# Performance work log

Measured on AMD Instinct MI355X. Metric: run time of the kernel, lower is better.

## Reference

```python
import jax, jax.numpy as jnp
import numpy as np

BIGNET_DIM = 1024
N_LAYERS = 18   # 6 blocks * 3 QLoRALinear
N_LN = 5
GROUPS = 64     # 1024 / group_size(16)
GS = 16
RANK = 32
BATCH = 16384
EPS = 1e-5


def dequant(qw, scale):
    # qw: [O, G, gs] int 0..15, scale: [O, G] per-group max-abs norm
    w = (qw.astype(jnp.float32) / 15.0 * 2.0 - 1.0) * scale[..., None]
    return w.reshape(qw.shape[0], -1)  # [O, I]


def qlora_linear(x, qw, scale, b, a_w, b_w):
    w = dequant(qw, scale)                      # [O, I]
    base = x @ w.T + b                          # [N, O]
    lora = (x @ a_w.T) @ b_w.T                  # [N, r] @ [r, O]
    return base + lora


def layernorm(h, g, b):
    mu = h.mean(-1, keepdims=True)
    var = jnp.mean((h - mu) ** 2, -1, keepdims=True)
    return (h - mu) * jax.lax.rsqrt(var + EPS) * g + b


def setup_inputs() -> dict:
    key = jax.random.key(0)
    ks = jax.random.split(key, 8)
    x = jax.random.normal(ks[0], (BATCH, BIGNET_DIM), jnp.float32)
    qw = jax.random.randint(ks[1], (N_LAYERS, BIGNET_DIM, GROUPS, GS), 0, 16, jnp.int32)
    scale = jax.random.uniform(ks[2], (N_LAYERS, BIGNET_DIM, GROUPS), jnp.float32) * 0.05
    bias = jax.random.normal(ks[3], (N_LAYERS, BIGNET_DIM), jnp.float32) * 0.02
    la = jax.random.normal(ks[4], (N_LAYERS, RANK, BIGNET_DIM), jnp.float32) * (2.0 / BIGNET_DIM) ** 0.5
    # note: torch zero-inits lora_b; use small random values so the LoRA path is testable
    lb = jax.random.normal(ks[5], (N_LAYERS, BIGNET_DIM, RANK), jnp.float32) * 0.01
    ln_w = jnp.ones((N_LN, BIGNET_DIM), jnp.float32)
    ln_b = jnp.zeros((N_LN, BIGNET_DIM), jnp.float32)
    return {"x": x, "scale": scale, "bias": bias, "la": la, "lb": lb,
            "ln_w": ln_w, "ln_b": ln_b, "qw": qw}


def reference(x, scale, bias, la, lb, ln_w, ln_b, qw):
    h = x
    li = 0
    for blk in range(6):
        r = h
        for j in range(3):
            h = qlora_linear(h, qw[li], scale[li], bias[li], la[li], lb[li])
            li += 1
            if j < 2:
                h = jax.nn.relu(h)
        h = h + r
        if blk < 5:
            h = layernorm(h, ln_w[blk], ln_b[blk])
    return h
```

## Files before the change

kernel.cpp:

```cpp
#include <hip/hip_runtime.h>

typedef unsigned short UST;
typedef __attribute__((ext_vector_type(8))) __bf16 bf16x8;
typedef __attribute__((ext_vector_type(4))) float f32x4;

__device__ __forceinline__ float bf2f(UST u) {
    union { unsigned int i; float f; } v; v.i = ((unsigned int)u) << 16; return v.f;
}
__device__ __forceinline__ UST f2bf(float f) {
    union { float f; unsigned int i; } v; v.f = f;
    return (UST)((v.i + 0x7fffu + ((v.i >> 16) & 1u)) >> 16);
}

__device__ __forceinline__ void gl2lds16(const UST* g, UST* l) {
    __builtin_amdgcn_global_load_lds(
        (const __attribute__((address_space(1))) unsigned int*)g,
        (__attribute__((address_space(3))) unsigned int*)l, 16, 0, 0);
}

#define WBAR8 asm volatile("s_waitcnt vmcnt(8)\n\ts_barrier" ::: "memory")
#define WBAR4 asm volatile("s_waitcnt vmcnt(4)\n\ts_barrier" ::: "memory")
#define WBAR0 asm volatile("s_waitcnt vmcnt(0)\n\ts_barrier" ::: "memory")
#define BAR   asm volatile("s_barrier" ::: "memory")
#define LGB   asm volatile("s_waitcnt lgkmcnt(0)\n\ts_barrier" ::: "memory")
#define LGW   do { asm volatile("s_waitcnt lgkmcnt(0)" ::: "memory"); \
                   __builtin_amdgcn_sched_barrier(0); } while (0)

__global__ __launch_bounds__(256) void prep_w(
    const int* __restrict__ qw, const float* __restrict__ scale,
    const float* __restrict__ la, const float* __restrict__ lb,
    UST* __restrict__ wp)
{
    int l = blockIdx.x, ot = blockIdx.y, it = blockIdx.z;
    __shared__ float buf[8192];
    __shared__ float sc_s[128 * 8];
    int t = threadIdx.x;
    int wave = t >> 6, lane = t & 63;
    int wm = wave >> 1, wn = wave & 1;
    int la15 = lane & 15, qa = lane >> 4;

    {
        int e = t * 4;
        int o = e >> 3, g = e & 7;
        const float* sb = scale + ((size_t)l * 1024 + ot * 128 + o) * 64 + it * 8 + g;
        *(float4*)&sc_s[e] = *(const float4*)sb;
    }

    float* last = buf;
    {
        const float* laB = la + (size_t)l * 32 * 1024 + it * 128;
        #pragma unroll
        for (int p = 0; p < 4; p++) {
            int e = t * 4 + p * 1024;
            int r = e >> 7, i0 = e & 127;
            float4 v = *(const float4*)(laB + (size_t)r * 1024 + i0);
            last[(i0 + 0) * 33 + r] = v.x;
            last[(i0 + 1) * 33 + r] = v.y;
            last[(i0 + 2) * 33 + r] = v.z;
            last[(i0 + 3) * 33 + r] = v.w;
        }
    }

    bf16x8 af[4];
    const float* lbL = lb + ((size_t)l * 1024 + ot * 128 + wm * 64 + la15) * 32 + qa * 8;
    #pragma unroll
    for (int mi = 0; mi < 4; mi++) {
        float4 u0 = *(const float4*)(lbL + mi * 16 * 32);
        float4 u1 = *(const float4*)(lbL + mi * 16 * 32 + 4);
        union { bf16x8 v; UST u[8]; } A;
        A.u[0] = f2bf(u0.x); A.u[1] = f2bf(u0.y); A.u[2] = f2bf(u0.z); A.u[3] = f2bf(u0.w);
        A.u[4] = f2bf(u1.x); A.u[5] = f2bf(u1.y); A.u[6] = f2bf(u1.z); A.u[7] = f2bf(u1.w);
        af[mi] = A.v;
    }

    __syncthreads();

    bf16x8 bfr[4];
    #pragma unroll
    for (int ni = 0; ni < 4; ni++) {
        int iloc = wn * 64 + ni * 16 + la15;
        const float* pp = &last[iloc * 33 + qa * 8];
        union { bf16x8 v; UST u[8]; } B;
        #pragma unroll
        for (int j = 0; j < 8; j++) B.u[j] = f2bf(pp[j]);
        bfr[ni] = B.v;
    }

    f32x4 acc[4][4];
    #pragma unroll
    for (int mi = 0; mi < 4; mi++)
        #pragma unroll
        for (int ni = 0; ni < 4; ni++) {
            acc[mi][ni] = (f32x4){0.f, 0.f, 0.f, 0.f};
            acc[mi][ni] = __builtin_amdgcn_mfma_f32_16x16x32_bf16(
                af[mi], bfr[ni], acc[mi][ni], 0, 0, 0);
        }

    __syncthreads();

    float* cs = buf;
    int cc = t & 15, rw = t >> 4;
    UST* wL = wp + (size_t)l * 1048576;
    const int* qL = qw + (size_t)l * 1048576;
    #pragma unroll
    for (int h = 0; h < 2; ++h) {
        int4 qd[4][2];
        #pragma unroll
        for (int g = 0; g < 4; g++) {
            int rl = g * 16 + rw;
            const int* qrow = qL + (size_t)(ot * 128 + h * 64 + rl) * 1024
                              + it * 128 + cc * 8;
            qd[g][0] = *(const int4*)qrow;
            qd[g][1] = *(const int4*)(qrow + 4);
        }
        if (wm == h) {
            #pragma unroll
            for (int mi = 0; mi < 4; mi++)
                #pragma unroll
                for (int ni = 0; ni < 4; ni++) {
                    int colx = (wn * 64 + ni * 16 + la15) ^ (qa << 4);
                    #pragma unroll
                    for (int r2 = 0; r2 < 4; r2++) {
                        int rl = mi * 16 + qa * 4 + r2;
                        cs[rl * 128 + colx] = acc[mi][ni][r2];
                    }
                }
        }
        LGB;
        #pragma unroll
        for (int g = 0; g < 4; ++g) {
            int rl = g * 16 + rw;
            int swz = ((rl >> 2) & 3) << 2;
            int gr0 = ((cc * 2) ^ swz) * 4;
            float4 v0 = *(const float4*)&cs[rl * 128 + gr0];
            float4 v1 = *(const float4*)&cs[rl * 128 + gr0 + 4];
            float s = sc_s[(h * 64 + rl) * 8 + (cc >> 1)];
            float t2 = s * (2.0f / 15.0f);
            float o0 = fmaf((float)qd[g][0].x, t2, v0.x - s);
            float o1 = fmaf((float)qd[g][0].y, t2, v0.y - s);
            float o2 = fmaf((float)qd[g][0].z, t2, v0.z - s);
            float o3 = fmaf((float)qd[g][0].w, t2, v0.w - s);
            float o4 = fmaf((float)qd[g][1].x, t2, v1.x - s);
            float o5 = fmaf((float)qd[g][1].y, t2, v1.y - s);
            float o6 = fmaf((float)qd[g][1].z, t2, v1.z - s);
            float o7 = fmaf((float)qd[g][1].w, t2, v1.w - s);
            uint4 pk;
            pk.x = (unsigned)f2bf(o0) | ((unsigned)f2bf(o1) << 16);
            pk.y = (unsigned)f2bf(o2) | ((unsigned)f2bf(o3) << 16);
            pk.z = (unsigned)f2bf(o4) | ((unsigned)f2bf(o5) << 16);
            pk.w = (unsigned)f2bf(o6) | ((unsigned)f2bf(o7) << 16);
            *(uint4*)&wL[(size_t)(ot * 128 + h * 64 + rl) * 1024 + it * 128 + cc * 8] = pk;
        }
        LGB;
    }
}

__global__ __launch_bounds__(256) void f32_to_bf16(const float* __restrict__ x,
                                                   UST* __restrict__ o)
{
    size_t i = ((size_t)blockIdx.x * 256 + threadIdx.x) * 4;
    float4 v = *(const float4*)(x + i);
    *(ushort4*)(o + i) = make_ushort4(f2bf(v.x), f2bf(v.y), f2bf(v.z), f2bf(v.w));
}

#define BK 32

__global__ __launch_bounds__(512, 2) void gemm_ep(
    const UST* __restrict__ X, const UST* __restrict__ W,
    const float* __restrict__ bias,
    UST* __restrict__ outb, const UST* __restrict__ resid,
    float* __restrict__ outf, int mode)
{
    const int K = 1024;
    __shared__ UST smem[65536];
    int tid = threadIdx.x;
    int wave = tid >> 6, lane = tid & 63;
    int wm = wave >> 2, wn = wave & 3;
    int la15 = lane & 15, qa = lane >> 4;

    int bid = blockIdx.x;
    int xcd = bid & 7, idx = bid >> 3;
    int bm = xcd * 8 + (idx & 7);
    int bn = idx >> 3;

    int c0 = tid, c1 = tid + 512;
    int r0 = c0 >> 2, k0c = ((c0 & 3) ^ ((r0 >> 1) & 3)) * 8;
    int r1 = c1 >> 2, k1c = ((c1 & 3) ^ ((r1 >> 1) & 3)) * 8;
    const UST* gA0 = X + (size_t)(bm * 256 + r0) * K + k0c;
    const UST* gA1 = X + (size_t)(bm * 256 + r1) * K + k1c;
    const UST* gB0 = W + (size_t)(bn * 256 + r0) * K + k0c;
    const UST* gB1 = W + (size_t)(bn * 256 + r1) * K + k1c;

    int offA[8], offB[4];
    #pragma unroll
    for (int i = 0; i < 8; i++) {
        int ra = wm * 128 + i * 16 + la15;
        offA[i] = ra * 32 + ((qa ^ ((ra >> 1) & 3)) * 8);
    }
    #pragma unroll
    for (int i = 0; i < 4; i++) {
        int rb = wn * 64 + i * 16 + la15;
        offB[i] = rb * 32 + ((qa ^ ((rb >> 1) & 3)) * 8);
    }

    f32x4 acc[8][4];
    #pragma unroll
    for (int i = 0; i < 8; i++)
        #pragma unroll
        for (int j = 0; j < 4; j++) acc[i][j] = (f32x4){0.f, 0.f, 0.f, 0.f};

    auto stageA = [&](int s) {
        UST* sA = smem + (s & 3) * 16384;
        gl2lds16(gA0 + s * BK, sA + c0 * 8);
        gl2lds16(gA1 + s * BK, sA + c1 * 8);
    };
    auto stageB = [&](int s) {
        UST* sB = smem + (s & 3) * 16384 + 8192;
        gl2lds16(gB0 + s * BK, sB + c0 * 8);
        gl2lds16(gB1 + s * BK, sB + c1 * 8);
    };

    stageA(0); stageB(0);
    stageA(1); stageB(1);
    stageA(2); stageB(2);

#define STEPBODY(s, WAITM, DOST)                                            \
    {                                                                       \
        const UST* pA = smem + ((s) & 3) * 16384;                           \
        const UST* pB = pA + 8192;                                          \
        WAITM;                                             \
        bf16x8 af0[4], bfn[4];                                              \
        _Pragma("unroll")                                                   \
        for (int mi = 0; mi < 4; mi++) af0[mi] = *(const bf16x8*)&pA[offA[mi]]; \
        _Pragma("unroll")                                                   \
        for (int ni = 0; ni < 4; ni++) bfn[ni] = *(const bf16x8*)&pB[offB[ni]]; \
        if (DOST) stageA((s) + 3);                                          \
        LGW;                                                                \
        __builtin_amdgcn_s_setprio(1);                                      \
        _Pragma("unroll")                                                   \
        for (int mi = 0; mi < 4; mi++)                                      \
            _Pragma("unroll")                                               \
            for (int ni = 0; ni < 4; ni++)                                  \
                acc[mi][ni] = __builtin_amdgcn_mfma_f32_16x16x32_bf16(      \
                    af0[mi], bfn[ni], acc[mi][ni], 0, 0, 0);                \
        __builtin_amdgcn_s_setprio(0);                                      \
        BAR;                                                                \
        bf16x8 af1[4];                                                      \
        _Pragma("unroll")                                                   \
        for (int mi = 0; mi < 4; mi++) af1[mi] = *(const bf16x8*)&pA[offA[4 + mi]]; \
        if (DOST) stageB((s) + 3);                                          \
        LGW;                                                                \
        __builtin_amdgcn_s_setprio(1);                                      \
        _Pragma("unroll")                                                   \
        for (int mi = 0; mi < 4; mi++)                                      \
            _Pragma("unroll")                                               \
            for (int ni = 0; ni < 4; ni++)                                  \
                acc[4 + mi][ni] = __builtin_amdgcn_mfma_f32_16x16x32_bf16(  \
                    af1[mi], bfn[ni], acc[4 + mi][ni], 0, 0, 0);            \
        __builtin_amdgcn_s_setprio(0);                                      \
    }

    for (int s = 0; s < 29; ++s) STEPBODY(s, WBAR8, 1);
    STEPBODY(29, WBAR8, 0);
    STEPBODY(30, WBAR4, 0);
    STEPBODY(31, WBAR0, 0);
#undef STEPBODY
    LGB;

    float* cs = (float*)smem;
    int cc = tid & 31, rw = tid >> 5;
    int gcolb = bn * 256 + cc * 8;
    float4 bv0 = *(const float4*)&bias[gcolb];
    float4 bv1 = *(const float4*)&bias[gcolb + 4];

    #pragma unroll
    for (int h = 0; h < 4; ++h) {
        if (wm == (h >> 1)) {
            #pragma unroll
            for (int m = 0; m < 4; m++) {
                int mi = (h & 1) * 4 + m;
                #pragma unroll
                for (int ni = 0; ni < 4; ni++) {
                    int colx = (wn * 64 + ni * 16 + la15) ^ (qa << 4);
                    #pragma unroll
                    for (int r2 = 0; r2 < 4; r2++) {
                        int rl = m * 16 + qa * 4 + r2;
                        cs[rl * 256 + colx] = acc[mi][ni][r2];
                    }
                }
            }
        }
        LGB;
        #pragma unroll
        for (int g = 0; g < 4; ++g) {
            int rl = g * 16 + rw;
            int swz = ((rl >> 2) & 3) << 2;
            int gr0 = ((cc * 2) ^ swz) * 4;
            float4 v0 = *(const float4*)&cs[rl * 256 + gr0];
            float4 v1 = *(const float4*)&cs[rl * 256 + gr0 + 4];
            float o0 = v0.x + bv0.x, o1 = v0.y + bv0.y;
            float o2 = v0.z + bv0.z, o3 = v0.w + bv0.w;
            float o4 = v1.x + bv1.x, o5 = v1.y + bv1.y;
            float o6 = v1.z + bv1.z, o7 = v1.w + bv1.w;
            if (mode == 0) {
                o0 = fmaxf(o0, 0.f); o1 = fmaxf(o1, 0.f);
                o2 = fmaxf(o2, 0.f); o3 = fmaxf(o3, 0.f);
                o4 = fmaxf(o4, 0.f); o5 = fmaxf(o5, 0.f);
                o6 = fmaxf(o6, 0.f); o7 = fmaxf(o7, 0.f);
            }
            int grow = bm * 256 + h * 64 + rl;
            size_t base = (size_t)grow * 1024 + gcolb;
            if (mode != 0) {
                ushort4 rv0 = *(const ushort4*)&resid[base];
                ushort4 rv1 = *(const ushort4*)&resid[base + 4];
                o0 += bf2f(rv0.x); o1 += bf2f(rv0.y);
                o2 += bf2f(rv0.z); o3 += bf2f(rv0.w);
                o4 += bf2f(rv1.x); o5 += bf2f(rv1.y);
                o6 += bf2f(rv1.z); o7 += bf2f(rv1.w);
            }
            if (mode == 2) {
                *(float4*)&outf[base] = make_float4(o0, o1, o2, o3);
                *(float4*)&outf[base + 4] = make_float4(o4, o5, o6, o7);
            } else {
                uint4 pk;
                pk.x = (unsigned)f2bf(o0) | ((unsigned)f2bf(o1) << 16);
                pk.y = (unsigned)f2bf(o2) | ((unsigned)f2bf(o3) << 16);
                pk.z = (unsigned)f2bf(o4) | ((unsigned)f2bf(o5) << 16);
                pk.w = (unsigned)f2bf(o6) | ((unsigned)f2bf(o7) << 16);
                *(uint4*)&outb[base] = pk;
            }
        }
        LGB;
    }
}

__global__ __launch_bounds__(256) void ln_only(
    const UST* __restrict__ s, UST* __restrict__ r,
    const float* __restrict__ g, const float* __restrict__ b)
{
    int wave = threadIdx.x >> 6, lane = threadIdx.x & 63;
    int row = blockIdx.x * 4 + wave;
    const UST* sp = s + (size_t)row * 1024;
    UST* rp = r + (size_t)row * 1024;

    float v[16];
    float sum = 0.f, ss = 0.f;
    #pragma unroll
    for (int k = 0; k < 4; k++) {
        ushort4 hv = *(const ushort4*)(sp + k * 256 + lane * 4);
        float a0 = bf2f(hv.x), a1 = bf2f(hv.y), a2 = bf2f(hv.z), a3 = bf2f(hv.w);
        v[k * 4 + 0] = a0; v[k * 4 + 1] = a1; v[k * 4 + 2] = a2; v[k * 4 + 3] = a3;
        sum += a0 + a1 + a2 + a3;
        ss += a0 * a0 + a1 * a1 + a2 * a2 + a3 * a3;
    }
    #pragma unroll
    for (int off = 32; off > 0; off >>= 1) {
        sum += __shfl_down(sum, off, 64);
        ss  += __shfl_down(ss, off, 64);
    }
    sum = __shfl(sum, 0, 64);
    ss  = __shfl(ss, 0, 64);
    float mean = sum * (1.0f / 1024.0f);
    float var = ss * (1.0f / 1024.0f) - mean * mean;
    float rstd = rsqrtf(var + 1e-5f);

    #pragma unroll
    for (int k = 0; k < 4; k++) {
        int c = k * 256 + lane * 4;
        float4 gv = *(const float4*)(g + c);
        float4 bv = *(const float4*)(b + c);
        ushort4 o;
        o.x = f2bf((v[k * 4 + 0] - mean) * rstd * gv.x + bv.x);
        o.y = f2bf((v[k * 4 + 1] - mean) * rstd * gv.y + bv.y);
        o.z = f2bf((v[k * 4 + 2] - mean) * rstd * gv.z + bv.z);
        o.w = f2bf((v[k * 4 + 3] - mean) * rstd * gv.w + bv.w);
        *(ushort4*)(rp + c) = o;
    }
}

extern "C" void kernel_launch(void* const* d_in, const int* in_sizes, int n_in,
                              void* d_out, int out_size, void* d_ws, size_t ws_size,
                              hipStream_t stream) {
    const float* x     = (const float*)d_in[0];
    const float* scale = (const float*)d_in[1];
    const float* bias  = (const float*)d_in[2];
    const float* la    = (const float*)d_in[3];
    const float* lb    = (const float*)d_in[4];
    const float* ln_w  = (const float*)d_in[5];
    const float* ln_b  = (const float*)d_in[6];
    const int*   qw    = (const int*)d_in[7];

    const int M = in_sizes[0] / 1024;
    const size_t WPB = (size_t)18 * 1024 * 1024 * 2;
    const size_t ACT = (size_t)M * 1024 * 2;

    UST* wp = (UST*)d_ws;
    UST* A  = (UST*)((char*)d_ws + WPB);
    UST* Cb = (UST*)((char*)d_ws + WPB + ACT);
    UST* Bb = (UST*)d_out;

    prep_w<<<dim3(18, 8, 8), 256, 0, stream>>>(qw, scale, la, lb, wp);
    f32_to_bf16<<<(M * 1024) / (256 * 4), 256, 0, stream>>>(x, A);

    int nblk = (M / 256) * 4;
    int li = 0;
    for (int blk = 0; blk < 6; ++blk) {
        gemm_ep<<<nblk, 512, 0, stream>>>(
            A, wp + (size_t)li * 1024 * 1024, bias + li * 1024, Bb, nullptr, nullptr, 0);
        li++;
        gemm_ep<<<nblk, 512, 0, stream>>>(
            Bb, wp + (size_t)li * 1024 * 1024, bias + li * 1024, Cb, nullptr, nullptr, 0);
        li++;
        if (blk < 5) {
            gemm_ep<<<nblk, 512, 0, stream>>>(
                Cb, wp + (size_t)li * 1024 * 1024, bias + li * 1024, Bb, A, nullptr, 1);
            li++;
            ln_only<<<M / 4, 256, 0, stream>>>(Bb, A, ln_w + blk * 1024, ln_b + blk * 1024);
        } else {
            gemm_ep<<<nblk, 512, 0, stream>>>(
                Cb, wp + (size_t)li * 1024 * 1024, bias + li * 1024, nullptr, A,
                (float*)d_out, 2);
            li++;
        }
    }
}
```

Baseline: 929.9 us.

## Prefetch next-stage LDS fragments into double-buffered registers during GEMM main loop

Restructures the GEMM main loop so that the B fragments and first half of the A fragments for the next K-step are read from LDS into ping-pong register sets while the current step's second MFMA half runs. All four global-to-LDS copies for a stage are now issued together, and the per-step barrier count drops from two to one at the end of each step. The goal is to hide LDS read latency behind MFMAs and cut synchronisation. In exchange it raises register pressure and makes the wait counts more delicate, since the loads for step s+3 now target the buffer just read in step s-1.

Result: slower. 1.035 ms (+11.3%).

```diff
diff --git a/kernel.cpp b/kernel.cpp
--- a/kernel.cpp
+++ b/kernel.cpp
@@ -18,10 +18,9 @@
         (__attribute__((address_space(3))) unsigned int*)l, 16, 0, 0);
 }
 
-#define WBAR8 asm volatile("s_waitcnt vmcnt(8)\n\ts_barrier" ::: "memory")
 #define WBAR4 asm volatile("s_waitcnt vmcnt(4)\n\ts_barrier" ::: "memory")
 #define WBAR0 asm volatile("s_waitcnt vmcnt(0)\n\ts_barrier" ::: "memory")
-#define BAR   asm volatile("s_barrier" ::: "memory")
+#define WNONE do {} while (0)
 #define LGB   asm volatile("s_waitcnt lgkmcnt(0)\n\ts_barrier" ::: "memory")
 #define LGW   do { asm volatile("s_waitcnt lgkmcnt(0)" ::: "memory"); \
                    __builtin_amdgcn_sched_barrier(0); } while (0)
@@ -209,63 +208,73 @@
         #pragma unroll
         for (int j = 0; j < 4; j++) acc[i][j] = (f32x4){0.f, 0.f, 0.f, 0.f};
 
-    auto stageA = [&](int s) {
-        UST* sA = smem + (s & 3) * 16384;
-        gl2lds16(gA0 + s * BK, sA + c0 * 8);
-        gl2lds16(gA1 + s * BK, sA + c1 * 8);
+    auto stage = [&](int s) {
+        UST* d = smem + (s & 3) * 16384;
+        gl2lds16(gA0 + s * BK, d + c0 * 8);
+        gl2lds16(gA1 + s * BK, d + c1 * 8);
+        gl2lds16(gB0 + s * BK, d + 8192 + c0 * 8);
+        gl2lds16(gB1 + s * BK, d + 8192 + c1 * 8);
     };
-    auto stageB = [&](int s) {
-        UST* sB = smem + (s & 3) * 16384 + 8192;
-        gl2lds16(gB0 + s * BK, sB + c0 * 8);
-        gl2lds16(gB1 + s * BK, sB + c1 * 8);
-    };
-
-    stageA(0); stageB(0);
-    stageA(1); stageB(1);
-    stageA(2); stageB(2);
-
-#define STEPBODY(s, WAITM, DOST)                                            \
+
+    bf16x8 bfA[4], af0A[4], bfB[4], af0B[4];
+
+    stage(0); stage(1); stage(2);
+    WBAR4;
+    {
+        const UST* pA = smem;
+        const UST* pB = pA + 8192;
+        #pragma unroll
+        for (int i = 0; i < 4; i++) bfA[i] = *(const bf16x8*)&pB[offB[i]];
+        #pragma unroll
+        for (int i = 0; i < 4; i++) af0A[i] = *(const bf16x8*)&pA[offA[i]];
+    }
+
+#define STEP(s, BF_C, AF0_C, BF_N, AF0_N, DOST, DONXT, WENDM)               \
     {                                                                       \
         const UST* pA = smem + ((s) & 3) * 16384;                           \
-        const UST* pB = pA + 8192;                                          \
-        WAITM;                                             \
-        bf16x8 af0[4], bfn[4];                                              \
+        const UST* pAn = smem + (((s) + 1) & 3) * 16384;                    \
+        const UST* pBn = pAn + 8192;                                        \
+        LGW;                                        \
+        bf16x8 af1[4];                                                      \
         _Pragma("unroll")                                                   \
-        for (int mi = 0; mi < 4; mi++) af0[mi] = *(const bf16x8*)&pA[offA[mi]]; \
-        _Pragma("unroll")                                                   \
-        for (int ni = 0; ni < 4; ni++) bfn[ni] = *(const bf16x8*)&pB[offB[ni]]; \
-        if (DOST) stageA((s) + 3);                                          \
-        LGW;                                                                \
+        for (int i = 0; i < 4; i++) af1[i] = *(const bf16x8*)&pA[offA[4 + i]]; \
+        if (DOST) stage((s) + 3);                                           \
         __builtin_amdgcn_s_setprio(1);                                      \
         _Pragma("unroll")                                                   \
         for (int mi = 0; mi < 4; mi++)                                      \
             _Pragma("unroll")                                               \
             for (int ni = 0; ni < 4; ni++)                                  \
                 acc[mi][ni] = __builtin_amdgcn_mfma_f32_16x16x32_bf16(      \
-                    af0[mi], bfn[ni], acc[mi][ni], 0, 0, 0);                \
+                    AF0_C[mi], BF_C[ni], acc[mi][ni], 0, 0, 0);             \
         __builtin_amdgcn_s_setprio(0);                                      \
-        BAR;                                                                \
-        bf16x8 af1[4];                                                      \
-        _Pragma("unroll")                                                   \
-        for (int mi = 0; mi < 4; mi++) af1[mi] = *(const bf16x8*)&pA[offA[4 + mi]]; \
-        if (DOST) stageB((s) + 3);                                          \
-        LGW;                                                                \
+        LGW;                                     \
+        if (DONXT) {                                                        \
+            _Pragma("unroll")                                               \
+            for (int i = 0; i < 4; i++) BF_N[i] = *(const bf16x8*)&pBn[offB[i]]; \
+            _Pragma("unroll")                                               \
+            for (int i = 0; i < 4; i++) AF0_N[i] = *(const bf16x8*)&pAn[offA[i]]; \
+        }                                                                   \
         __builtin_amdgcn_s_setprio(1);                                      \
         _Pragma("unroll")                                                   \
         for (int mi = 0; mi < 4; mi++)                                      \
             _Pragma("unroll")                                               \
             for (int ni = 0; ni < 4; ni++)                                  \
                 acc[4 + mi][ni] = __builtin_amdgcn_mfma_f32_16x16x32_bf16(  \
-                    af1[mi], bfn[ni], acc[4 + mi][ni], 0, 0, 0);            \
+                    af1[mi], BF_C[ni], acc[4 + mi][ni], 0, 0, 0);           \
         __builtin_amdgcn_s_setprio(0);                                      \
-    }
-
-    for (int s = 0; s < 29; ++s) STEPBODY(s, WBAR8, 1);
-    STEPBODY(29, WBAR8, 0);
-    STEPBODY(30, WBAR4, 0);
-    STEPBODY(31, WBAR0, 0);
-#undef STEPBODY
-    LGB;
+        WENDM;                                                              \
+    }
+
+    #pragma unroll 2
+    for (int s = 0; s < 28; s += 2) {
+        STEP(s, bfA, af0A, bfB, af0B, 1, 1, WBAR4);
+        STEP(s + 1, bfB, af0B, bfA, af0A, 1, 1, WBAR4);
+    }
+    STEP(28, bfA, af0A, bfB, af0B, 1, 1, WBAR4);
+    STEP(29, bfB, af0B, bfA, af0A, 0, 1, WBAR0);
+    STEP(30, bfA, af0A, bfB, af0B, 0, 1, WBAR0);
+    STEP(31, bfB, af0B, bfA, af0A, 0, 0, WNONE);
+#undef STEP
 
     float* cs = (float*)smem;
     int cc = tid & 31, rw = tid >> 5;
```

## Restructure GEMM main loop to BK=64 double-buffered half-tile staging

Applied to the files above, without the earlier changes.

Replaces the 4-stage BK=32 pipeline in the GEMM kernel with a 2-buffer BK=64 scheme. Each buffer is loaded as four 128-row quarter tiles (A halves, B halves) that are staged one at a time, interleaved with the four MFMA sub-blocks of the previous tile. The LDS swizzle changes to an 8-slot XOR pattern for 64-wide rows. The aim is fewer barrier and wait rounds per K element and finer-grained overlap of global-to-LDS loads with compute. In exchange it adds more barriers per group and a shallower prefetch distance, which may expose load latency.

New measurement: 915.7 us. Within noise of the previous version (-1.5%).

```diff
diff --git a/kernel.cpp b/kernel.cpp
--- a/kernel.cpp
+++ b/kernel.cpp
@@ -18,13 +18,13 @@
         (__attribute__((address_space(3))) unsigned int*)l, 16, 0, 0);
 }
 
-#define WBAR8 asm volatile("s_waitcnt vmcnt(8)\n\ts_barrier" ::: "memory")
-#define WBAR4 asm volatile("s_waitcnt vmcnt(4)\n\ts_barrier" ::: "memory")
-#define WBAR0 asm volatile("s_waitcnt vmcnt(0)\n\ts_barrier" ::: "memory")
-#define BAR   asm volatile("s_barrier" ::: "memory")
-#define LGB   asm volatile("s_waitcnt lgkmcnt(0)\n\ts_barrier" ::: "memory")
-#define LGW   do { asm volatile("s_waitcnt lgkmcnt(0)" ::: "memory"); \
-                   __builtin_amdgcn_sched_barrier(0); } while (0)
+#define LGB asm volatile("s_waitcnt lgkmcnt(0)\n\ts_barrier" ::: "memory")
+#define LGW do { asm volatile("s_waitcnt lgkmcnt(0)" ::: "memory"); \
+                 __builtin_amdgcn_sched_barrier(0); } while (0)
+#define BARR __builtin_amdgcn_s_barrier()
+#define EW2 asm volatile("s_waitcnt vmcnt(2)" ::: "memory")
+#define EW0 asm volatile("s_waitcnt vmcnt(0)" ::: "memory")
+#define EWN do {} while (0)
 
 __global__ __launch_bounds__(256) void prep_w(
     const int* __restrict__ qw, const float* __restrict__ scale,
@@ -163,7 +163,7 @@
     *(ushort4*)(o + i) = make_ushort4(f2bf(v.x), f2bf(v.y), f2bf(v.z), f2bf(v.w));
 }
 
-#define BK 32
+#define BKT 64
 
 __global__ __launch_bounds__(512, 2) void gemm_ep(
     const UST* __restrict__ X, const UST* __restrict__ W,
@@ -183,24 +183,30 @@
     int bm = xcd * 8 + (idx & 7);
     int bn = idx >> 3;
 
-    int c0 = tid, c1 = tid + 512;
-    int r0 = c0 >> 2, k0c = ((c0 & 3) ^ ((r0 >> 1) & 3)) * 8;
-    int r1 = c1 >> 2, k1c = ((c1 & 3) ^ ((r1 >> 1) & 3)) * 8;
-    const UST* gA0 = X + (size_t)(bm * 256 + r0) * K + k0c;
-    const UST* gA1 = X + (size_t)(bm * 256 + r1) * K + k1c;
-    const UST* gB0 = W + (size_t)(bn * 256 + r0) * K + k0c;
-    const UST* gB1 = W + (size_t)(bn * 256 + r1) * K + k1c;
-
-    int offA[8], offB[4];
-    #pragma unroll
-    for (int i = 0; i < 8; i++) {
-        int ra = wm * 128 + i * 16 + la15;
-        offA[i] = ra * 32 + ((qa ^ ((ra >> 1) & 3)) * 8);
-    }
-    #pragma unroll
-    for (int i = 0; i < 4; i++) {
-        int rb = wn * 64 + i * 16 + la15;
-        offB[i] = rb * 32 + ((qa ^ ((rb >> 1) & 3)) * 8);
+    const UST* srcA[2];
+    const UST* srcB[2];
+    int dstc[2];
+    #pragma unroll
+    for (int j = 0; j < 2; j++) {
+        int c = tid + j * 512;
+        int row = c >> 3, sl = c & 7;
+        int kof = (sl ^ (row & 7)) * 8;
+        srcA[j] = X + (size_t)(bm * 256 + row) * K + kof;
+        srcB[j] = W + (size_t)(bn * 256 + row) * K + kof;
+        dstc[j] = c * 8;
+    }
+
+    int offA[2][4], offB[2][4];
+    #pragma unroll
+    for (int kk = 0; kk < 2; kk++) {
+        #pragma unroll
+        for (int i = 0; i < 4; i++) {
+            int rih = i * 16 + la15;
+            offA[kk][i] = wm * 8192 + rih * 64 + (((kk * 4 + qa) ^ (rih & 7)) * 8);
+            int cih = (wn & 1) * 64 + i * 16 + la15;
+            offB[kk][i] = 16384 + (wn >> 1) * 8192 + cih * 64
+                          + (((kk * 4 + qa) ^ (cih & 7)) * 8);
+        }
     }
 
     f32x4 acc[8][4];
@@ -209,63 +215,78 @@
         #pragma unroll
         for (int j = 0; j < 4; j++) acc[i][j] = (f32x4){0.f, 0.f, 0.f, 0.f};
 
-    auto stageA = [&](int s) {
-        UST* sA = smem + (s & 3) * 16384;
-        gl2lds16(gA0 + s * BK, sA + c0 * 8);
-        gl2lds16(gA1 + s * BK, sA + c1 * 8);
+    auto stageH = [&](int t, int H) {
+        UST* dst = smem + ((t & 1) * 32768 + H * 8192);
+        #pragma unroll
+        for (int j = 0; j < 2; j++) {
+            const UST* src = (H < 2 ? srcA[j] : srcB[j])
+                             + (size_t)(H & 1) * (128 * 1024) + t * BKT;
+            gl2lds16(src, dst + dstc[j]);
+        }
     };
-    auto stageB = [&](int s) {
-        UST* sB = smem + (s & 3) * 16384 + 8192;
-        gl2lds16(gB0 + s * BK, sB + c0 * 8);
-        gl2lds16(gB1 + s * BK, sB + c1 * 8);
-    };
-
-    stageA(0); stageB(0);
-    stageA(1); stageB(1);
-    stageA(2); stageB(2);
-
-#define STEPBODY(s, WAITM, DOST)                                            \
+
+#define MF16(Q)                                                             \
+    _Pragma("unroll")                                                       \
+    for (int m = 0; m < 4; m++)                                             \
+        _Pragma("unroll")                                                   \
+        for (int n = 0; n < 4; n++)                                         \
+            acc[(Q) * 4 + m][n] = __builtin_amdgcn_mfma_f32_16x16x32_bf16(  \
+                af[m], bfr[n], acc[(Q) * 4 + m][n], 0, 0, 0)
+
+#define GROUP(T, SP, SN, EW)                                                \
     {                                                                       \
-        const UST* pA = smem + ((s) & 3) * 16384;                           \
-        const UST* pB = pA + 8192;                                          \
-        WAITM;                                             \
-        bf16x8 af0[4], bfn[4];                                              \
-        _Pragma("unroll")                                                   \
-        for (int mi = 0; mi < 4; mi++) af0[mi] = *(const bf16x8*)&pA[offA[mi]]; \
-        _Pragma("unroll")                                                   \
-        for (int ni = 0; ni < 4; ni++) bfn[ni] = *(const bf16x8*)&pB[offB[ni]]; \
-        if (DOST) stageA((s) + 3);                                          \
-        LGW;                                                                \
-        __builtin_amdgcn_s_setprio(1);                                      \
-        _Pragma("unroll")                                                   \
-        for (int mi = 0; mi < 4; mi++)                                      \
-            _Pragma("unroll")                                               \
-            for (int ni = 0; ni < 4; ni++)                                  \
-                acc[mi][ni] = __builtin_amdgcn_mfma_f32_16x16x32_bf16(      \
-                    af0[mi], bfn[ni], acc[mi][ni], 0, 0, 0);                \
-        __builtin_amdgcn_s_setprio(0);                                      \
-        BAR;                                                                \
-        bf16x8 af1[4];                                                      \
-        _Pragma("unroll")                                                   \
-        for (int mi = 0; mi < 4; mi++) af1[mi] = *(const bf16x8*)&pA[offA[4 + mi]]; \
-        if (DOST) stageB((s) + 3);                                          \
-        LGW;                                                                \
-        __builtin_amdgcn_s_setprio(1);                                      \
-        _Pragma("unroll")                                                   \
-        for (int mi = 0; mi < 4; mi++)                                      \
-            _Pragma("unroll")                                               \
-            for (int ni = 0; ni < 4; ni++)                                  \
-                acc[4 + mi][ni] = __builtin_amdgcn_mfma_f32_16x16x32_bf16(  \
-                    af1[mi], bfn[ni], acc[4 + mi][ni], 0, 0, 0);            \
-        __builtin_amdgcn_s_setprio(0);                                      \
-    }
-
-    for (int s = 0; s < 29; ++s) STEPBODY(s, WBAR8, 1);
-    STEPBODY(29, WBAR8, 0);
-    STEPBODY(30, WBAR4, 0);
-    STEPBODY(31, WBAR0, 0);
-#undef STEPBODY
-    LGB;
+        const UST* p = smem + ((T) & 1) * 32768;                            \
+        bf16x8 af[4], bfr[4];                                               \
+                                                         \
+        _Pragma("unroll")                                                   \
+        for (int i = 0; i < 4; i++) bfr[i] = *(const bf16x8*)&p[offB[0][i]];\
+        _Pragma("unroll")                                                   \
+        for (int i = 0; i < 4; i++) af[i] = *(const bf16x8*)&p[offA[0][i]]; \
+        if (SP) stageH((T) + 1, 3);                                         \
+        BARR; LGW;                                                          \
+        __builtin_amdgcn_s_setprio(1); MF16(0); __builtin_amdgcn_s_setprio(0); \
+        BARR;                                                               \
+                                                         \
+        _Pragma("unroll")                                                   \
+        for (int i = 0; i < 4; i++)                                         \
+            af[i] = *(const bf16x8*)&p[offA[0][i] + 4096];                  \
+        if (SP) stageH((T) + 1, 0);                                         \
+        BARR; LGW;                                                          \
+        __builtin_amdgcn_s_setprio(1); MF16(1); __builtin_amdgcn_s_setprio(0); \
+        BARR;                                                               \
+                             \
+        _Pragma("unroll")                                                   \
+        for (int i = 0; i < 4; i++) bfr[i] = *(const bf16x8*)&p[offB[1][i]];\
+        _Pragma("unroll")                                                   \
+        for (int i = 0; i < 4; i++) af[i] = *(const bf16x8*)&p[offA[1][i]]; \
+        if (SP) stageH((T) + 1, 1);                                         \
+        BARR; LGW;                                                          \
+        __builtin_amdgcn_s_setprio(1); MF16(0); __builtin_amdgcn_s_setprio(0); \
+        BARR;                                                               \
+                             \
+        _Pragma("unroll")                                                   \
+        for (int i = 0; i < 4; i++)                                         \
+            af[i] = *(const bf16x8*)&p[offA[1][i] + 4096];                  \
+        if (SN) stageH((T) + 2, 2);                                         \
+        BARR; LGW;                                                          \
+        __builtin_amdgcn_s_setprio(1); MF16(1); __builtin_amdgcn_s_setprio(0); \
+        EW;                                                                 \
+        BARR;                                                               \
+    }
+
+    #pragma unroll
+    for (int H = 0; H < 4; H++) stageH(0, H);
+    #pragma unroll
+    for (int H = 0; H < 4; H++) stageH(1, H);
+    asm volatile("s_waitcnt vmcnt(8)" ::: "memory");
+    BARR;
+
+    GROUP(0, 0, 1, EW2);
+    for (int g = 1; g <= 13; ++g) GROUP(g, 1, 1, EW2);
+    GROUP(14, 1, 0, EW0);
+    GROUP(15, 0, 0, EWN);
+#undef GROUP
+#undef MF16
 
     float* cs = (float*)smem;
     int cc = tid & 31, rw = tid >> 5;
```
